# Kernel tuning notes

Measured on AMD Instinct MI355X. Metric: run time of the kernel, lower is better.

## Reference

```python
import jax, jax.numpy as jnp
import numpy as np

B, T, S, E, D = 16, 1024, 1024, 1024, 1024  # batch, trg_len, src_len, enc_dim, trg_dim

def setup_inputs() -> dict:
    key = jax.random.key(0)
    k1, k2, k3, k4, k5 = jax.random.split(key, 5)
    sc = 0.02
    return {
        "hidden": jax.random.normal(k1, (B, T, D), dtype=jnp.float32),
        "encoder_outputs": jax.random.normal(k2, (B, S, E), dtype=jnp.float32),
        "W_attn": jax.random.normal(k3, (D, E), dtype=jnp.float32) * sc,
        "b_attn": jax.random.normal(k4, (D,), dtype=jnp.float32) * sc,
        "W_out": jax.random.normal(k5, (D, E + D), dtype=jnp.float32) * sc,
    }

def reference(hidden, encoder_outputs, W_attn, b_attn, W_out):
    # score, method='general': energies = Linear(enc_out) ; bmm(hidden, energies^T)
    proj = jnp.einsum('bse,de->bsd', encoder_outputs, W_attn) + b_attn  # (B,S,D)
    attn_energies = jnp.einsum('btd,bsd->bts', hidden, proj)            # (B,T,S)
    attn_weights = jax.nn.softmax(attn_energies, axis=-1)               # (B,T,S)
    weighted_context = jnp.einsum('bts,bse->bte', attn_weights, encoder_outputs)  # (B,T,E)
    h_cat = jnp.concatenate([weighted_context, hidden], axis=-1)        # (B,T,E+D)
    h_tilde = jnp.tanh(jnp.einsum('btc,dc->btd', h_cat, W_out))         # (B,T,D)
    return h_tilde, attn_weights, attn_energies
```

## Files before the change

### kernel.cpp

```cpp
#include <hip/hip_runtime.h>
#include <stdint.h>


typedef __bf16 bf16x8 __attribute__((ext_vector_type(8)));
typedef float  f32x4  __attribute__((ext_vector_type(4)));

enum { MODE_PROJ = 0, MODE_ENERGY = 1, MODE_WC = 2, MODE_OUT = 3 };

__device__ __forceinline__ ushort f2bf(float f) {
    uint32_t u = __builtin_bit_cast(uint32_t, f);
    u += 0x7fffu + ((u >> 16) & 1u);
    return (ushort)(u >> 16);
}

#define GLB_PTR(p) ((const __attribute__((address_space(1))) void*)(p))
#define LDS_PTR(p) ((__attribute__((address_space(3))) void*)(p))

__device__ __forceinline__ void stage_tile(const ushort* __restrict__ g, int ld,
                                           ushort* lds, int wave, int lane) {
#pragma unroll
    for (int i = 0; i < 4; ++i) {
        const int seg  = i * 4 + wave;
        const int p    = seg * 1024 + lane * 16;
        const int row  = p >> 7;
        const int cpos = (p >> 4) & 7;
        const int csrc = cpos ^ (row & 7);
        const ushort* gp = g + (size_t)row * ld + csrc * 8;
        __builtin_amdgcn_global_load_lds(GLB_PTR(gp), LDS_PTR((char*)lds + seg * 1024), 16, 0, 0);
    }
}

template <int MODE>
__global__ __launch_bounds__(256) void gemm_bt(
    const ushort* __restrict__ A0, const ushort* __restrict__ A1,
    const ushort* __restrict__ B0, const float* __restrict__ bias,
    ushort* __restrict__ out_bf, float* __restrict__ out_f)
{
    constexpr int    KTOT   = (MODE == MODE_OUT) ? 2048 : 1024;
    constexpr int    LDB    = (MODE == MODE_OUT) ? 2048 : 1024;
    constexpr size_t BBATCH = (MODE == MODE_ENERGY || MODE == MODE_WC) ? ((size_t)1 << 20) : 0;

    const int b    = blockIdx.z;
    const int bm   = blockIdx.y * 128;
    const int bn   = blockIdx.x * 128;
    const int wave = threadIdx.x >> 6;
    const int lane = threadIdx.x & 63;
    const int wm   = wave >> 1;
    const int wn   = wave & 1;

    const ushort* Ab0 = A0 + ((size_t)b << 20) + (size_t)bm * 1024;
    const ushort* Ab1 = nullptr;
    if constexpr (MODE == MODE_OUT) Ab1 = A1 + ((size_t)b << 20) + (size_t)bm * 1024;
    const ushort* Bb0 = B0 + (size_t)b * BBATCH + (size_t)bn * LDB;

    __shared__ ushort ldsA[128 * 64];
    __shared__ ushort ldsB[128 * 64];

    f32x4 acc[4][4];
#pragma unroll
    for (int r = 0; r < 4; ++r)
#pragma unroll
        for (int c = 0; c < 4; ++c) acc[r][c] = f32x4{0.f, 0.f, 0.f, 0.f};

    for (int k0 = 0; k0 < KTOT; k0 += 64) {
        const ushort* Ag; int kA;
        if constexpr (MODE == MODE_OUT) { Ag = (k0 < 1024) ? Ab0 : Ab1; kA = k0 & 1023; }
        else                            { Ag = Ab0;                     kA = k0; }

        __syncthreads();
        stage_tile(Ag + kA, 1024, ldsA, wave, lane);
        stage_tile(Bb0 + k0, LDB,  ldsB, wave, lane);
        __syncthreads();

#pragma unroll
        for (int ks = 0; ks < 2; ++ks) {
            const int quad = lane >> 4;
            const int l15  = lane & 15;
            bf16x8 af[4], bfr[4];
#pragma unroll
            for (int r = 0; r < 4; ++r) {
                const int row   = wm * 64 + r * 16 + l15;
                const int chunk = ks * 4 + quad;
                af[r] = *(const bf16x8*)&ldsA[row * 64 + ((chunk ^ (row & 7)) * 8)];
            }
#pragma unroll
            for (int c = 0; c < 4; ++c) {
                const int row   = wn * 64 + c * 16 + l15;
                const int chunk = ks * 4 + quad;
                bfr[c] = *(const bf16x8*)&ldsB[row * 64 + ((chunk ^ (row & 7)) * 8)];
            }
#pragma unroll
            for (int r = 0; r < 4; ++r)
#pragma unroll
                for (int c = 0; c < 4; ++c)
                    acc[r][c] = __builtin_amdgcn_mfma_f32_16x16x32_bf16(af[r], bfr[c], acc[r][c], 0, 0, 0);
        }
    }

    const size_t obase = (size_t)b << 20;
    const int quad = lane >> 4;
    const int l15  = lane & 15;
#pragma unroll
    for (int r = 0; r < 4; ++r) {
#pragma unroll
        for (int c = 0; c < 4; ++c) {
#pragma unroll
            for (int g = 0; g < 4; ++g) {
                const int row = bm + wm * 64 + r * 16 + quad * 4 + g;
                const int col = bn + wn * 64 + c * 16 + l15;
                float v = acc[r][c][g];
                const size_t idx = obase + (size_t)row * 1024 + col;
                if constexpr (MODE == MODE_PROJ) {
                    out_bf[idx] = f2bf(v + bias[col]);
                } else if constexpr (MODE == MODE_ENERGY) {
                    out_f[idx] = v;
                } else if constexpr (MODE == MODE_WC) {
                    out_bf[idx] = f2bf(v);
                } else {
                    out_f[idx] = tanhf(v);
                }
            }
        }
    }
}

__global__ __launch_bounds__(256) void conv_k(const float* __restrict__ in,
                                              ushort* __restrict__ out) {
    const size_t i = (size_t)blockIdx.x * 256 + threadIdx.x;
    float4 v = ((const float4*)in)[i];
    ushort4 o;
    o.x = f2bf(v.x); o.y = f2bf(v.y); o.z = f2bf(v.z); o.w = f2bf(v.w);
    ((ushort4*)out)[i] = o;
}

__global__ __launch_bounds__(256) void transconv_k(const float* __restrict__ in,
                                                   ushort* __restrict__ out) {
    __shared__ ushort t[64][65];
    const int b  = blockIdx.z;
    const int s0 = blockIdx.y * 64, e0 = blockIdx.x * 64;
    const float* ip = in  + ((size_t)b << 20);
    ushort*      op = out + ((size_t)b << 20);
    const int tx = threadIdx.x & 15;
    const int ty = threadIdx.x >> 4;
#pragma unroll
    for (int i = 0; i < 4; ++i) {
        const int s = ty + i * 16;
        float4 v = *(const float4*)&ip[(size_t)(s0 + s) * 1024 + e0 + tx * 4];
        t[tx * 4 + 0][s] = f2bf(v.x); t[tx * 4 + 1][s] = f2bf(v.y);
        t[tx * 4 + 2][s] = f2bf(v.z); t[tx * 4 + 3][s] = f2bf(v.w);
    }
    __syncthreads();
#pragma unroll
    for (int i = 0; i < 4; ++i) {
        const int e = ty + i * 16;
        ushort4 v;
        v.x = t[e][tx * 4 + 0]; v.y = t[e][tx * 4 + 1];
        v.z = t[e][tx * 4 + 2]; v.w = t[e][tx * 4 + 3];
        *(ushort4*)&op[(size_t)(e0 + e) * 1024 + s0 + tx * 4] = v;
    }
}

__global__ __launch_bounds__(256) void softmax_k(const float* __restrict__ en,
                                                 float* __restrict__ w,
                                                 ushort* __restrict__ wbf) {
    const size_t row = blockIdx.x;
    const float* e = en + (row << 10);
    const int tid = threadIdx.x;
    const int wv = tid >> 6, ln = tid & 63;

    float4 v = ((const float4*)e)[tid];
    float m = fmaxf(fmaxf(v.x, v.y), fmaxf(v.z, v.w));
#pragma unroll
    for (int o = 32; o; o >>= 1) m = fmaxf(m, __shfl_xor(m, o, 64));
    __shared__ float sm[4];
    if (!ln) sm[wv] = m;
    __syncthreads();
    m = fmaxf(fmaxf(sm[0], sm[1]), fmaxf(sm[2], sm[3]));

    const float e0 = expf(v.x - m), e1 = expf(v.y - m), e2 = expf(v.z - m), e3 = expf(v.w - m);
    float s = e0 + e1 + e2 + e3;
#pragma unroll
    for (int o = 32; o; o >>= 1) s += __shfl_xor(s, o, 64);
    __shared__ float ss[4];
    if (!ln) ss[wv] = s;
    __syncthreads();
    s = ss[0] + ss[1] + ss[2] + ss[3];
    const float inv = 1.0f / s;

    const float w0 = e0 * inv, w1 = e1 * inv, w2 = e2 * inv, w3 = e3 * inv;
    ((float4*)(w + (row << 10)))[tid] = float4{w0, w1, w2, w3};
    ushort4 o4;
    o4.x = f2bf(w0); o4.y = f2bf(w1); o4.z = f2bf(w2); o4.w = f2bf(w3);
    ((ushort4*)(wbf + (row << 10)))[tid] = o4;
}

extern "C" void kernel_launch(void* const* d_in, const int* in_sizes, int n_in,
                              void* d_out, int out_size, void* d_ws, size_t ws_size,
                              hipStream_t stream) {
    (void)in_sizes; (void)n_in; (void)out_size; (void)ws_size;
    const float* hidden = (const float*)d_in[0];
    const float* enc    = (const float*)d_in[1];
    const float* Wattn  = (const float*)d_in[2];
    const float* battn  = (const float*)d_in[3];
    const float* Wout   = (const float*)d_in[4];

    const size_t M16 = (size_t)16 * 1024 * 1024;
    float* out_h = (float*)d_out;
    float* out_w = out_h + M16;
    float* out_e = out_w + M16;

    ushort* ws = (ushort*)d_ws;
    ushort* hidden_bf = ws;
    ushort* encwc_bf  = ws + M16;
    ushort* proj_bf   = ws + 2 * M16;
    ushort* wattn_bf  = ws + 3 * M16;
    ushort* wout_bf   = ws + 3 * M16 + (1u << 20);
    ushort* encT_bf   = (ushort*)out_h;
    ushort* weights_bf = (ushort*)out_h + M16;

    dim3 blk(256, 1, 1);
    dim3 gG(8, 8, 16);
    dim3 gT(16, 16, 16);

    conv_k<<<dim3(16384), blk, 0, stream>>>(hidden, hidden_bf);
    conv_k<<<dim3(16384), blk, 0, stream>>>(enc, encwc_bf);
    conv_k<<<dim3(1024),  blk, 0, stream>>>(Wattn, wattn_bf);
    conv_k<<<dim3(2048),  blk, 0, stream>>>(Wout, wout_bf);
    transconv_k<<<gT, blk, 0, stream>>>(enc, encT_bf);
    gemm_bt<MODE_PROJ><<<gG, blk, 0, stream>>>(encwc_bf, nullptr, wattn_bf, battn,
                                               proj_bf, nullptr);
    gemm_bt<MODE_ENERGY><<<gG, blk, 0, stream>>>(hidden_bf, nullptr, proj_bf, nullptr,
                                                 nullptr, out_e);
    softmax_k<<<dim3(16 * 1024), blk, 0, stream>>>(out_e, out_w, weights_bf);
    gemm_bt<MODE_WC><<<gG, blk, 0, stream>>>(weights_bf, nullptr, encT_bf, nullptr,
                                             encwc_bf, nullptr);
    gemm_bt<MODE_OUT><<<gG, blk, 0, stream>>>(encwc_bf, hidden_bf, wout_bf, nullptr,
                                              nullptr, out_h);
}
```

Measured before the change: 618.4 us.

## Double-buffer GEMM LDS tiles, remap blocks for XCD locality, fuse enc conversions

The GEMM kernel now uses two LDS buffers so the async global-to-LDS load of the next K tile overlaps MFMA compute on the current one, with one barrier per step instead of two. Block indices are remapped so consecutive hardware-dispatched blocks on an XCD share a batch and its tiles, aiming for better L2 reuse. The transpose-convert kernel also writes the non-transposed bf16 copy of encoder_outputs, which removes one full conversion pass over enc. Doubling the LDS footprint may reduce occupancy.

```diff
diff --git a/kernel.cpp b/kernel.cpp
--- a/kernel.cpp
+++ b/kernel.cpp
@@ -38,11 +38,15 @@
 {
     constexpr int    KTOT   = (MODE == MODE_OUT) ? 2048 : 1024;
     constexpr int    LDB    = (MODE == MODE_OUT) ? 2048 : 1024;
+    constexpr int    NT     = KTOT / 64;
     constexpr size_t BBATCH = (MODE == MODE_ENERGY || MODE == MODE_WC) ? ((size_t)1 << 20) : 0;
 
-    const int b    = blockIdx.z;
-    const int bm   = blockIdx.y * 128;
-    const int bn   = blockIdx.x * 128;
+    const int flat = (blockIdx.z * 8 + blockIdx.y) * 8 + blockIdx.x;
+    const int nid  = ((flat & 7) << 7) | (flat >> 3);
+    const int b    = nid >> 6;
+    const int bm   = ((nid >> 3) & 7) << 7;
+    const int bn   = (nid & 7) << 7;
+
     const int wave = threadIdx.x >> 6;
     const int lane = threadIdx.x & 63;
     const int wm   = wave >> 1;
@@ -53,8 +57,8 @@
     if constexpr (MODE == MODE_OUT) Ab1 = A1 + ((size_t)b << 20) + (size_t)bm * 1024;
     const ushort* Bb0 = B0 + (size_t)b * BBATCH + (size_t)bn * LDB;
 
-    __shared__ ushort ldsA[128 * 64];
-    __shared__ ushort ldsB[128 * 64];
+    __shared__ ushort ldsA[2][128 * 64];
+    __shared__ ushort ldsB[2][128 * 64];
 
     f32x4 acc[4][4];
 #pragma unroll
@@ -62,16 +66,16 @@
 #pragma unroll
         for (int c = 0; c < 4; ++c) acc[r][c] = f32x4{0.f, 0.f, 0.f, 0.f};
 
-    for (int k0 = 0; k0 < KTOT; k0 += 64) {
+    auto stage_step = [&](int t, int buf) {
+        const int k0 = t * 64;
         const ushort* Ag; int kA;
         if constexpr (MODE == MODE_OUT) { Ag = (k0 < 1024) ? Ab0 : Ab1; kA = k0 & 1023; }
         else                            { Ag = Ab0;                     kA = k0; }
-
-        __syncthreads();
-        stage_tile(Ag + kA, 1024, ldsA, wave, lane);
-        stage_tile(Bb0 + k0, LDB,  ldsB, wave, lane);
-        __syncthreads();
-
+        stage_tile(Ag + kA, 1024, ldsA[buf], wave, lane);
+        stage_tile(Bb0 + k0, LDB,  ldsB[buf], wave, lane);
+    };
+
+    auto compute_step = [&](int buf) {
 #pragma unroll
         for (int ks = 0; ks < 2; ++ks) {
             const int quad = lane >> 4;
@@ -81,13 +85,13 @@
             for (int r = 0; r < 4; ++r) {
                 const int row   = wm * 64 + r * 16 + l15;
                 const int chunk = ks * 4 + quad;
-                af[r] = *(const bf16x8*)&ldsA[row * 64 + ((chunk ^ (row & 7)) * 8)];
+                af[r] = *(const bf16x8*)&ldsA[buf][row * 64 + ((chunk ^ (row & 7)) * 8)];
             }
 #pragma unroll
             for (int c = 0; c < 4; ++c) {
                 const int row   = wn * 64 + c * 16 + l15;
                 const int chunk = ks * 4 + quad;
-                bfr[c] = *(const bf16x8*)&ldsB[row * 64 + ((chunk ^ (row & 7)) * 8)];
+                bfr[c] = *(const bf16x8*)&ldsB[buf][row * 64 + ((chunk ^ (row & 7)) * 8)];
             }
 #pragma unroll
             for (int r = 0; r < 4; ++r)
@@ -95,6 +99,18 @@
                 for (int c = 0; c < 4; ++c)
                     acc[r][c] = __builtin_amdgcn_mfma_f32_16x16x32_bf16(af[r], bfr[c], acc[r][c], 0, 0, 0);
         }
+    };
+
+    stage_step(0, 0);
+    __syncthreads();
+
+    for (int t = 0; t < NT; t += 2) {
+        stage_step(t + 1, 1);
+        compute_step(0);
+        __syncthreads();
+        if (t + 2 < NT) stage_step(t + 2, 0);
+        compute_step(1);
+        __syncthreads();
     }
 
     const size_t obase = (size_t)b << 20;
@@ -134,20 +150,25 @@
 }
 
 __global__ __launch_bounds__(256) void transconv_k(const float* __restrict__ in,
-                                                   ushort* __restrict__ out) {
+                                                   ushort* __restrict__ outT,
+                                                   ushort* __restrict__ outN) {
     __shared__ ushort t[64][65];
     const int b  = blockIdx.z;
     const int s0 = blockIdx.y * 64, e0 = blockIdx.x * 64;
-    const float* ip = in  + ((size_t)b << 20);
-    ushort*      op = out + ((size_t)b << 20);
+    const float* ip = in   + ((size_t)b << 20);
+    ushort*      tp = outT + ((size_t)b << 20);
+    ushort*      np = outN + ((size_t)b << 20);
     const int tx = threadIdx.x & 15;
     const int ty = threadIdx.x >> 4;
 #pragma unroll
     for (int i = 0; i < 4; ++i) {
         const int s = ty + i * 16;
         float4 v = *(const float4*)&ip[(size_t)(s0 + s) * 1024 + e0 + tx * 4];
-        t[tx * 4 + 0][s] = f2bf(v.x); t[tx * 4 + 1][s] = f2bf(v.y);
-        t[tx * 4 + 2][s] = f2bf(v.z); t[tx * 4 + 3][s] = f2bf(v.w);
+        ushort4 n4;
+        n4.x = f2bf(v.x); n4.y = f2bf(v.y); n4.z = f2bf(v.z); n4.w = f2bf(v.w);
+        *(ushort4*)&np[(size_t)(s0 + s) * 1024 + e0 + tx * 4] = n4;
+        t[tx * 4 + 0][s] = n4.x; t[tx * 4 + 1][s] = n4.y;
+        t[tx * 4 + 2][s] = n4.z; t[tx * 4 + 3][s] = n4.w;
     }
     __syncthreads();
 #pragma unroll
@@ -156,7 +177,7 @@
         ushort4 v;
         v.x = t[e][tx * 4 + 0]; v.y = t[e][tx * 4 + 1];
         v.z = t[e][tx * 4 + 2]; v.w = t[e][tx * 4 + 3];
-        *(ushort4*)&op[(size_t)(e0 + e) * 1024 + s0 + tx * 4] = v;
+        *(ushort4*)&tp[(size_t)(e0 + e) * 1024 + s0 + tx * 4] = v;
     }
 }
 
@@ -223,10 +244,9 @@
     dim3 gT(16, 16, 16);
 
     conv_k<<<dim3(16384), blk, 0, stream>>>(hidden, hidden_bf);
-    conv_k<<<dim3(16384), blk, 0, stream>>>(enc, encwc_bf);
     conv_k<<<dim3(1024),  blk, 0, stream>>>(Wattn, wattn_bf);
     conv_k<<<dim3(2048),  blk, 0, stream>>>(Wout, wout_bf);
-    transconv_k<<<gT, blk, 0, stream>>>(enc, encT_bf);
+    transconv_k<<<gT, blk, 0, stream>>>(enc, encT_bf, encwc_bf);
     gemm_bt<MODE_PROJ><<<gG, blk, 0, stream>>>(encwc_bf, nullptr, wattn_bf, battn,
                                                proj_bf, nullptr);
     gemm_bt<MODE_ENERGY><<<gG, blk, 0, stream>>>(hidden_bf, nullptr, proj_bf, nullptr,
```

Result: faster. 581.3 us (-6.0%).
